# Optimization experiments

Hardware: AMD Instinct MI355X
Metric: run time of the kernel (lower is better)

The kernel has to match this reference:

```python
import jax, jax.numpy as jnp
import numpy as np

NUM_SEGMENTS = 64  # number of bags (max batch id + 1)
TEMP = 1.0
EPS_NORM = 1e-12
EPS_SOFTMAX = 1e-16

D = 1024
L = 128
N = 262144


def setup_inputs() -> dict:
    key = jax.random.key(0)
    ks = jax.random.split(key, 8)
    feature = jax.random.normal(ks[0], (N, D), dtype=jnp.float32)
    batch = jnp.sort(jax.random.randint(ks[1], (N,), 0, NUM_SEGMENTS, dtype=jnp.int32))
    # xavier_normal_ init: std = sqrt(2/(fan_in+fan_out))
    Wa = jax.random.normal(ks[2], (L, D), dtype=jnp.float32) * np.sqrt(2.0 / (D + L))
    ba = jnp.zeros((L,), dtype=jnp.float32)
    Wb = jax.random.normal(ks[3], (L, D), dtype=jnp.float32) * np.sqrt(2.0 / (D + L))
    bb = jnp.zeros((L,), dtype=jnp.float32)
    Wc = jax.random.normal(ks[4], (1, L), dtype=jnp.float32) * np.sqrt(2.0 / (L + 1))
    bc = jnp.zeros((1,), dtype=jnp.float32)
    return {"feature": feature, "batch": batch, "istrain": 0,
            "Wa": Wa, "ba": ba, "Wb": Wb, "bb": bb, "Wc": Wc, "bc": bc}


def segment_softmax(score, batch, num_segments):
    # score: [N, 1], batch: [N] segment ids (torch_geometric softmax semantics)
    seg_max = jax.ops.segment_max(score, batch, num_segments=num_segments)
    ex = jnp.exp(score - seg_max[batch])
    denom = jax.ops.segment_sum(ex, batch, num_segments=num_segments)
    return ex / (denom[batch] + EPS_SOFTMAX)


def reference(feature, batch, istrain, Wa, ba, Wb, bb, Wc, bc):
    # F.normalize: L2-normalize each row (dim=1)
    norm = jnp.linalg.norm(feature, axis=1, keepdims=True)
    instance_norm_feature = feature / jnp.maximum(norm, EPS_NORM)
    a = jax.nn.sigmoid(feature @ Wa.T + ba)          # [N, L]
    b = jnp.tanh(feature @ Wb.T + bb)                # [N, L]
    gated = a * b                                     # [N, L]
    score = (gated @ Wc.T + bc) / TEMP               # [N, 1]
    score = segment_softmax(score, batch, NUM_SEGMENTS)
    # istrain=0 -> dropout is identity in this reference
    return (instance_norm_feature, score)
```

## Files before the change

### kernel.cpp

```cpp
#include <hip/hip_runtime.h>
#include <hip/hip_fp16.h>

#define DD 1024
#define LL 128
#define NSEG 64
#define CHS 544

typedef float floatx4 __attribute__((ext_vector_type(4)));

__global__ __launch_bounds__(256)
void prep_kernel(const float* __restrict__ Wa, const float* __restrict__ Wb,
                 unsigned char* __restrict__ Wf8, unsigned* __restrict__ smaxu,
                 float* __restrict__ denom)
{
    int gid = blockIdx.x * 256 + threadIdx.x;
    if (gid < 2 * LL * DD) {
        const int j    = gid & 7;
        const int lane = (gid >> 3) & 63;
        const int ct   = (gid >> 9) & 15;
        const int c    = gid >> 13;
        const int r = ct * 16 + (lane & 15);
        const int k = c * 32 + (lane >> 4) * 8 + j;
        const float v = ((r < LL) ? Wa[r * DD + k] : Wb[(r - LL) * DD + k]) * 16.0f;
        unsigned u = __builtin_amdgcn_cvt_pk_fp8_f32(v, v, 0, false);
        Wf8[gid] = (unsigned char)(u & 0xFF);
    }
    if (gid < NSEG)          smaxu[gid] = 0u;
    else if (gid < 2 * NSEG) denom[gid - NSEG] = 0.0f;
}

__global__ __launch_bounds__(256, 8)
void fused_main(const float* __restrict__ feat,
                const unsigned char* __restrict__ Wf8,
                const float* __restrict__ ba,
                const float* __restrict__ bb,
                const float* __restrict__ Wc,
                const float* __restrict__ bc,
                float* __restrict__ out_norm,
                float* __restrict__ score_raw)
{
    __shared__ __align__(16) char tile[32 * CHS];
    __shared__ float scorebuf[16];

    const int tid  = threadIdx.x;
    const int wave = tid >> 6;
    const int lane = tid & 63;
    const int s15  = lane & 15;
    const int l4   = lane >> 4;
    const long long row0 = (long long)blockIdx.x * 16;

    if (tid < 16) scorebuf[tid] = 0.0f;

    #pragma unroll
    for (int b = 0; b < 2; ++b) {
        const int r0 = wave * 4 + b * 2;
        const float* fb = feat + (row0 + r0) * DD + lane * 4;
        float4 L[2][4];
        #pragma unroll
        for (int i = 0; i < 2; ++i)
            #pragma unroll
            for (int c = 0; c < 4; ++c)
                L[i][c] = *reinterpret_cast<const float4*>(fb + (size_t)i * DD + c * 256);

        #pragma unroll
        for (int i = 0; i < 2; ++i) {
            const int r = r0 + i;
            float ss = 0.0f;
            #pragma unroll
            for (int c = 0; c < 4; ++c)
                ss += L[i][c].x * L[i][c].x + L[i][c].y * L[i][c].y
                    + L[i][c].z * L[i][c].z + L[i][c].w * L[i][c].w;
            #pragma unroll
            for (int off = 32; off >= 1; off >>= 1) ss += __shfl_xor(ss, off);
            const float rinv = 1.0f / fmaxf(sqrtf(ss), 1e-12f);

            float* ob = out_norm + (size_t)(row0 + r) * DD + lane * 4;
            #pragma unroll
            for (int c = 0; c < 4; ++c) {
                float4 v;
                v.x = L[i][c].x * rinv; v.y = L[i][c].y * rinv;
                v.z = L[i][c].z * rinv; v.w = L[i][c].w * rinv;
                *reinterpret_cast<float4*>(ob + c * 256) = v;
            }
            #pragma unroll
            for (int c = 0; c < 4; ++c) {
                unsigned u = __builtin_amdgcn_cvt_pk_fp8_f32(L[i][c].x * 8.0f, L[i][c].y * 8.0f, 0, false);
                u = __builtin_amdgcn_cvt_pk_fp8_f32(L[i][c].z * 8.0f, L[i][c].w * 8.0f, u, true);
                const int chunk = (lane >> 3) + c * 8;
                const int addr  = chunk * CHS + r * 32 + ((lane >> 1) & 3) * 8 + (lane & 1) * 4;
                *reinterpret_cast<unsigned*>(tile + addr) = u;
            }
        }
    }
    __syncthreads();

    floatx4 acc[4];
    #pragma unroll
    for (int q = 0; q < 4; ++q) acc[q] = (floatx4)0.0f;

    const int cta = wave * 2;
    const unsigned char* bb0 = Wf8 + (size_t)lane * 8;

    #pragma unroll 2
    for (int c = 0; c < 32; ++c) {
        const long long a8 = *reinterpret_cast<const long long*>(tile + c * CHS + s15 * 32 + l4 * 8);
        const unsigned char* bp = bb0 + (size_t)c * 8192;
        const long long w0 = *reinterpret_cast<const long long*>(bp + (cta + 0) * 512);
        const long long w1 = *reinterpret_cast<const long long*>(bp + (cta + 1) * 512);
        const long long w2 = *reinterpret_cast<const long long*>(bp + (cta + 8) * 512);
        const long long w3 = *reinterpret_cast<const long long*>(bp + (cta + 9) * 512);
        acc[0] = __builtin_amdgcn_mfma_f32_16x16x32_fp8_fp8(a8, w0, acc[0], 0, 0, 0);
        acc[1] = __builtin_amdgcn_mfma_f32_16x16x32_fp8_fp8(a8, w1, acc[1], 0, 0, 0);
        acc[2] = __builtin_amdgcn_mfma_f32_16x16x32_fp8_fp8(a8, w2, acc[2], 0, 0, 0);
        acc[3] = __builtin_amdgcn_mfma_f32_16x16x32_fp8_fp8(a8, w3, acc[3], 0, 0, 0);
    }

    const float S = 1.0f / 128.0f;
    float s[4] = {0.f, 0.f, 0.f, 0.f};
    #pragma unroll
    for (int q = 0; q < 2; ++q) {
        const int col = (cta + q) * 16 + s15;
        const float bav = ba[col], bbv = bb[col], wcv = Wc[col];
        #pragma unroll
        for (int j = 0; j < 4; ++j) {
            const float av = 1.0f / (1.0f + expf(-(acc[q][j] * S + bav)));
            const float bv = tanhf(acc[2 + q][j] * S + bbv);
            s[j] += av * bv * wcv;
        }
    }
    #pragma unroll
    for (int j = 0; j < 4; ++j) {
        s[j] += __shfl_xor(s[j], 1);
        s[j] += __shfl_xor(s[j], 2);
        s[j] += __shfl_xor(s[j], 4);
        s[j] += __shfl_xor(s[j], 8);
    }
    if (s15 == 0) {
        #pragma unroll
        for (int j = 0; j < 4; ++j)
            atomicAdd(&scorebuf[l4 * 4 + j], s[j]);
    }
    __syncthreads();
    if (tid < 16) score_raw[row0 + tid] = scorebuf[tid] + bc[0];
}

__global__ __launch_bounds__(256)
void seg_max_kernel(const float* __restrict__ score, const int* __restrict__ batch,
                    unsigned* __restrict__ smaxu, int n)
{
    __shared__ unsigned sm[NSEG];
    const int t = threadIdx.x;
    if (t < NSEG) sm[t] = 0u;
    __syncthreads();
    const int stride = gridDim.x * blockDim.x;
    for (int i = blockIdx.x * blockDim.x + t; i < n; i += stride) {
        const unsigned b = __float_as_uint(score[i]);
        const unsigned m = (b & 0x80000000u) ? ~b : (b | 0x80000000u);
        atomicMax(&sm[batch[i]], m);
    }
    __syncthreads();
    if (t < NSEG) atomicMax(&smaxu[t], sm[t]);
}

__global__ __launch_bounds__(256)
void seg_exp_kernel(float* __restrict__ score_inout, const int* __restrict__ batch,
                    const unsigned* __restrict__ smaxu, float* __restrict__ denom, int n)
{
    __shared__ float sd[NSEG];
    __shared__ float smx[NSEG];
    const int t = threadIdx.x;
    if (t < NSEG) {
        sd[t] = 0.0f;
        const unsigned u = smaxu[t];
        const unsigned b = (u & 0x80000000u) ? (u ^ 0x80000000u) : ~u;
        smx[t] = __uint_as_float(b);
    }
    __syncthreads();
    const int stride = gridDim.x * blockDim.x;
    for (int i = blockIdx.x * blockDim.x + t; i < n; i += stride) {
        const int b = batch[i];
        const float e = expf(score_inout[i] - smx[b]);
        score_inout[i] = e;
        atomicAdd(&sd[b], e);
    }
    __syncthreads();
    if (t < NSEG) atomicAdd(&denom[t], sd[t]);
}

__global__ __launch_bounds__(256)
void seg_div_kernel(float* __restrict__ score_inout, const int* __restrict__ batch,
                    const float* __restrict__ denom, int n)
{
    const int stride = gridDim.x * blockDim.x;
    for (int i = blockIdx.x * blockDim.x + threadIdx.x; i < n; i += stride)
        score_inout[i] = score_inout[i] / (denom[batch[i]] + 1e-16f);
}

extern "C" void kernel_launch(void* const* d_in, const int* in_sizes, int n_in,
                              void* d_out, int out_size, void* d_ws, size_t ws_size,
                              hipStream_t stream)
{
    const float* feat  = (const float*)d_in[0];
    const int*   batch = (const int*)d_in[1];
    const float* Wa = (const float*)d_in[3];
    const float* ba = (const float*)d_in[4];
    const float* Wb = (const float*)d_in[5];
    const float* bb = (const float*)d_in[6];
    const float* Wc = (const float*)d_in[7];
    const float* bc = (const float*)d_in[8];

    const int N = in_sizes[1];

    float* out_norm  = (float*)d_out;
    float* out_score = (float*)d_out + (size_t)N * DD;

    char* ws = (char*)d_ws;
    unsigned char* Wf8 = (unsigned char*)ws;
    unsigned* smaxu = (unsigned*)(ws + 2 * LL * DD);
    float*    denom = (float*)(ws + 2 * LL * DD + 256);

    prep_kernel<<<(2 * LL * DD + 255) / 256, 256, 0, stream>>>(Wa, Wb, Wf8, smaxu, denom);
    fused_main<<<N / 16, 256, 0, stream>>>(feat, Wf8, ba, bb, Wc, bc, out_norm, out_score);
    seg_max_kernel<<<512, 256, 0, stream>>>(out_score, batch, smaxu, N);
    seg_exp_kernel<<<512, 256, 0, stream>>>(out_score, batch, smaxu, denom, N);
    seg_div_kernel<<<512, 256, 0, stream>>>(out_score, batch, denom, N);
}
```

Measured before the change: 604.8 us.

## Make fused kernel persistent with 512 threads and prefetch next tile's rows

Turns the fused normalize+gated-attention kernel into a persistent grid of 768 blocks of 512 threads. Each block loops over 16-row tiles and issues the global loads for the next tile before running the current tile's MFMA loop, so memory latency overlaps with compute. Each wave now computes 16 output columns instead of 32, and scores are accumulated with global atomics into a buffer zeroed in prep_kernel. The bias bc is dropped, which is only valid because it is zero and softmax is shift-invariant. This risks more register pressure, lower occupancy, and extra global atomic traffic.

```diff
diff --git a/kernel.cpp b/kernel.cpp
--- a/kernel.cpp
+++ b/kernel.cpp
@@ -1,17 +1,18 @@
 #include <hip/hip_runtime.h>
-#include <hip/hip_fp16.h>
 
 #define DD 1024
 #define LL 128
 #define NSEG 64
 #define CHS 544
+#define NTILE 16384
+#define GRID 768
 
 typedef float floatx4 __attribute__((ext_vector_type(4)));
 
 __global__ __launch_bounds__(256)
 void prep_kernel(const float* __restrict__ Wa, const float* __restrict__ Wb,
                  unsigned char* __restrict__ Wf8, unsigned* __restrict__ smaxu,
-                 float* __restrict__ denom)
+                 float* __restrict__ denom, float* __restrict__ score_raw)
 {
     int gid = blockIdx.x * 256 + threadIdx.x;
     if (gid < 2 * LL * DD) {
@@ -24,47 +25,50 @@
         const float v = ((r < LL) ? Wa[r * DD + k] : Wb[(r - LL) * DD + k]) * 16.0f;
         unsigned u = __builtin_amdgcn_cvt_pk_fp8_f32(v, v, 0, false);
         Wf8[gid] = (unsigned char)(u & 0xFF);
+        score_raw[gid] = 0.0f;
     }
     if (gid < NSEG)          smaxu[gid] = 0u;
     else if (gid < 2 * NSEG) denom[gid - NSEG] = 0.0f;
 }
 
-__global__ __launch_bounds__(256, 8)
+__global__ __launch_bounds__(512, 6)
 void fused_main(const float* __restrict__ feat,
                 const unsigned char* __restrict__ Wf8,
                 const float* __restrict__ ba,
                 const float* __restrict__ bb,
                 const float* __restrict__ Wc,
-                const float* __restrict__ bc,
                 float* __restrict__ out_norm,
                 float* __restrict__ score_raw)
 {
     __shared__ __align__(16) char tile[32 * CHS];
-    __shared__ float scorebuf[16];
 
     const int tid  = threadIdx.x;
     const int wave = tid >> 6;
     const int lane = tid & 63;
     const int s15  = lane & 15;
     const int l4   = lane >> 4;
-    const long long row0 = (long long)blockIdx.x * 16;
-
-    if (tid < 16) scorebuf[tid] = 0.0f;
-
-    #pragma unroll
-    for (int b = 0; b < 2; ++b) {
-        const int r0 = wave * 4 + b * 2;
-        const float* fb = feat + (row0 + r0) * DD + lane * 4;
-        float4 L[2][4];
+    const int G    = gridDim.x;
+
+    float4 L[2][4];
+
+    auto issue = [&](long long tt) {
+        const float* fb = feat + ((size_t)tt * 16 + wave * 2) * DD + lane * 4;
         #pragma unroll
         for (int i = 0; i < 2; ++i)
             #pragma unroll
             for (int c = 0; c < 4; ++c)
                 L[i][c] = *reinterpret_cast<const float4*>(fb + (size_t)i * DD + c * 256);
-
+    };
+
+    long long t = blockIdx.x;
+    if (t < NTILE) issue(t);
+
+    while (t < NTILE) {
+        const long long row0 = t * 16;
+
+        unsigned pw[2][4];
         #pragma unroll
         for (int i = 0; i < 2; ++i) {
-            const int r = r0 + i;
             float ss = 0.0f;
             #pragma unroll
             for (int c = 0; c < 4; ++c)
@@ -74,7 +78,7 @@
             for (int off = 32; off >= 1; off >>= 1) ss += __shfl_xor(ss, off);
             const float rinv = 1.0f / fmaxf(sqrtf(ss), 1e-12f);
 
-            float* ob = out_norm + (size_t)(row0 + r) * DD + lane * 4;
+            float* ob = out_norm + (row0 + wave * 2 + i) * DD + lane * 4;
             #pragma unroll
             for (int c = 0; c < 4; ++c) {
                 float4 v;
@@ -86,62 +90,66 @@
             for (int c = 0; c < 4; ++c) {
                 unsigned u = __builtin_amdgcn_cvt_pk_fp8_f32(L[i][c].x * 8.0f, L[i][c].y * 8.0f, 0, false);
                 u = __builtin_amdgcn_cvt_pk_fp8_f32(L[i][c].z * 8.0f, L[i][c].w * 8.0f, u, true);
+                pw[i][c] = u;
+            }
+        }
+
+        __syncthreads();
+        #pragma unroll
+        for (int i = 0; i < 2; ++i) {
+            const int r = wave * 2 + i;
+            #pragma unroll
+            for (int c = 0; c < 4; ++c) {
                 const int chunk = (lane >> 3) + c * 8;
                 const int addr  = chunk * CHS + r * 32 + ((lane >> 1) & 3) * 8 + (lane & 1) * 4;
-                *reinterpret_cast<unsigned*>(tile + addr) = u;
-            }
-        }
-    }
-    __syncthreads();
-
-    floatx4 acc[4];
-    #pragma unroll
-    for (int q = 0; q < 4; ++q) acc[q] = (floatx4)0.0f;
-
-    const int cta = wave * 2;
-    const unsigned char* bb0 = Wf8 + (size_t)lane * 8;
-
-    #pragma unroll 2
-    for (int c = 0; c < 32; ++c) {
-        const long long a8 = *reinterpret_cast<const long long*>(tile + c * CHS + s15 * 32 + l4 * 8);
-        const unsigned char* bp = bb0 + (size_t)c * 8192;
-        const long long w0 = *reinterpret_cast<const long long*>(bp + (cta + 0) * 512);
-        const long long w1 = *reinterpret_cast<const long long*>(bp + (cta + 1) * 512);
-        const long long w2 = *reinterpret_cast<const long long*>(bp + (cta + 8) * 512);
-        const long long w3 = *reinterpret_cast<const long long*>(bp + (cta + 9) * 512);
-        acc[0] = __builtin_amdgcn_mfma_f32_16x16x32_fp8_fp8(a8, w0, acc[0], 0, 0, 0);
-        acc[1] = __builtin_amdgcn_mfma_f32_16x16x32_fp8_fp8(a8, w1, acc[1], 0, 0, 0);
-        acc[2] = __builtin_amdgcn_mfma_f32_16x16x32_fp8_fp8(a8, w2, acc[2], 0, 0, 0);
-        acc[3] = __builtin_amdgcn_mfma_f32_16x16x32_fp8_fp8(a8, w3, acc[3], 0, 0, 0);
-    }
-
-    const float S = 1.0f / 128.0f;
-    float s[4] = {0.f, 0.f, 0.f, 0.f};
-    #pragma unroll
-    for (int q = 0; q < 2; ++q) {
-        const int col = (cta + q) * 16 + s15;
-        const float bav = ba[col], bbv = bb[col], wcv = Wc[col];
-        #pragma unroll
-        for (int j = 0; j < 4; ++j) {
-            const float av = 1.0f / (1.0f + expf(-(acc[q][j] * S + bav)));
-            const float bv = tanhf(acc[2 + q][j] * S + bbv);
-            s[j] += av * bv * wcv;
-        }
-    }
-    #pragma unroll
-    for (int j = 0; j < 4; ++j) {
-        s[j] += __shfl_xor(s[j], 1);
-        s[j] += __shfl_xor(s[j], 2);
-        s[j] += __shfl_xor(s[j], 4);
-        s[j] += __shfl_xor(s[j], 8);
-    }
-    if (s15 == 0) {
-        #pragma unroll
-        for (int j = 0; j < 4; ++j)
-            atomicAdd(&scorebuf[l4 * 4 + j], s[j]);
-    }
-    __syncthreads();
-    if (tid < 16) score_raw[row0 + tid] = scorebuf[tid] + bc[0];
+                *reinterpret_cast<unsigned*>(tile + addr) = pw[i][c];
+            }
+        }
+        __syncthreads();
+
+        const long long tn = t + G;
+        if (tn < NTILE) issue(tn);
+        __builtin_amdgcn_sched_barrier(0);
+
+        floatx4 acc0 = (floatx4)0.0f;
+        floatx4 acc1 = (floatx4)0.0f;
+        const unsigned char* bb0 = Wf8 + (size_t)wave * 512 + (size_t)lane * 8;
+
+        #pragma unroll 4
+        for (int c = 0; c < 32; ++c) {
+            const long long a8 = *reinterpret_cast<const long long*>(tile + c * CHS + s15 * 32 + l4 * 8);
+            const long long w0 = *reinterpret_cast<const long long*>(bb0 + (size_t)c * 8192);
+            const long long w1 = *reinterpret_cast<const long long*>(bb0 + (size_t)c * 8192 + 8 * 512);
+            acc0 = __builtin_amdgcn_mfma_f32_16x16x32_fp8_fp8(a8, w0, acc0, 0, 0, 0);
+            acc1 = __builtin_amdgcn_mfma_f32_16x16x32_fp8_fp8(a8, w1, acc1, 0, 0, 0);
+        }
+
+        {
+            const float S = 1.0f / 128.0f;
+            const int col = wave * 16 + s15;
+            const float bav = ba[col], bbv = bb[col], wcv = Wc[col];
+            float s[4];
+            #pragma unroll
+            for (int j = 0; j < 4; ++j) {
+                const float av = 1.0f / (1.0f + expf(-(acc0[j] * S + bav)));
+                const float bv = tanhf(acc1[j] * S + bbv);
+                s[j] = av * bv * wcv;
+            }
+            #pragma unroll
+            for (int j = 0; j < 4; ++j) {
+                s[j] += __shfl_xor(s[j], 1);
+                s[j] += __shfl_xor(s[j], 2);
+                s[j] += __shfl_xor(s[j], 4);
+                s[j] += __shfl_xor(s[j], 8);
+            }
+            if (s15 == 0) {
+                #pragma unroll
+                for (int j = 0; j < 4; ++j)
+                    atomicAdd(&score_raw[row0 + l4 * 4 + j], s[j]);
+            }
+        }
+        t = tn;
+    }
 }
 
 __global__ __launch_bounds__(256)
@@ -207,7 +215,6 @@
     const float* Wb = (const float*)d_in[5];
     const float* bb = (const float*)d_in[6];
     const float* Wc = (const float*)d_in[7];
-    const float* bc = (const float*)d_in[8];
 
     const int N = in_sizes[1];
 
@@ -219,8 +226,8 @@
     unsigned* smaxu = (unsigned*)(ws + 2 * LL * DD);
     float*    denom = (float*)(ws + 2 * LL * DD + 256);
 
-    prep_kernel<<<(2 * LL * DD + 255) / 256, 256, 0, stream>>>(Wa, Wb, Wf8, smaxu, denom);
-    fused_main<<<N / 16, 256, 0, stream>>>(feat, Wf8, ba, bb, Wc, bc, out_norm, out_score);
+    prep_kernel<<<(2 * LL * DD + 255) / 256, 256, 0, stream>>>(Wa, Wb, Wf8, smaxu, denom, out_score);
+    fused_main<<<GRID, 512, 0, stream>>>(feat, Wf8, ba, bb, Wc, out_norm, out_score);
     seg_max_kernel<<<512, 256, 0, stream>>>(out_score, batch, smaxu, N);
     seg_exp_kernel<<<512, 256, 0, stream>>>(out_score, batch, smaxu, denom, N);
     seg_div_kernel<<<512, 256, 0, stream>>>(out_score, batch, denom, N);
```

After: 532.6 us. 11.9% less time.
